# Performance work log

Measured on AMD Instinct MI355X. Metric: run time of the kernel, lower is better.

The kernel has to match this reference:

```python
import jax, jax.numpy as jnp
import numpy as np

NEG_BIG = -2.0**32 + 1.0  # padding value used by the torch module


def setup_inputs() -> dict:
    key = jax.random.key(0)
    k1, k2, k3, k4 = jax.random.split(key, 4)
    B, T, D = 8, 1024, 1024
    x = jax.random.normal(k1, (B, T, D), dtype=jnp.float32)
    mask = jnp.ones((B, T), dtype=jnp.float32)
    Wq = jax.random.normal(k2, (D, D), dtype=jnp.float32) * 0.02
    Wk = jax.random.normal(k3, (D, D), dtype=jnp.float32) * 0.02
    Wv = jax.random.normal(k4, (D, D), dtype=jnp.float32) * 0.02
    return {"x": x, "mask": mask, "Wq": Wq, "Wk": Wk, "Wv": Wv}


def reference(x, mask, Wq, Wk, Wv):
    # direction = FORWARD, dropout = 0.0, n_heads = 8
    n_heads = 8
    B, T, D = x.shape
    d = D // n_heads

    # nn.Linear(bias=False): y = x @ W.T
    Q = x @ Wq.T
    K = x @ Wk.T
    V = x @ Wv.T

    # torch.cat(torch.split(Q, d, dim=2), dim=0) -> [h*B, T, d], head-major
    def heads(t):
        return t.reshape(B, T, n_heads, d).transpose(2, 0, 1, 3)  # (h,B,T,d)

    Qh, Kh, Vh = heads(Q), heads(K), heads(V)

    scores = jnp.einsum('hbqd,hbkd->hbqk', Qh, Kh) / jnp.sqrt(jnp.float32(d))

    # key padding mask from K_ itself
    key_masks = jnp.sign(jnp.sum(jnp.abs(Kh), axis=-1))  # (h,B,T)
    scores = jnp.where(key_masks[:, :, None, :] == 0, jnp.float32(NEG_BIG), scores)

    # FORWARD direction: sw_col[i,j]=i, sw_row[i,j]=j; mask = (j > i) -> strict upper tri
    dir_mask = jnp.triu(jnp.ones((T, T), dtype=jnp.float32), k=1)
    adder = (1.0 - dir_mask) * -10000.0
    scores = scores + adder  # broadcasts over (h,B)

    attn = jax.nn.softmax(scores, axis=-1)

    query_masks = jnp.sign(jnp.sum(jnp.abs(Qh), axis=-1))  # (h,B,T)
    attn = attn * query_masks[:, :, :, None]

    out = jnp.einsum('hbqk,hbkd->hbqd', attn, Vh)  # (h,B,T,d)
    out = out.transpose(1, 2, 0, 3).reshape(B, T, D)  # cat heads back on feature dim

    out = out * mask[:, :, None]
    return out
```

## Files before the change

### kernel.cpp

```cpp
#include <hip/hip_runtime.h>
#include <hip/hip_bf16.h>
#include <stdint.h>


typedef __attribute__((ext_vector_type(8))) short short8;
typedef __attribute__((ext_vector_type(4))) float floatx4;

__device__ __forceinline__ short f2bf(float f) {
    union { float f; uint32_t u; } v; v.f = f;
    uint32_t r = v.u + 0x7fffu + ((v.u >> 16) & 1u);
    return (short)(r >> 16);
}

__device__ __forceinline__ void load_lds_16B(const void* g, void* l) {
    __builtin_amdgcn_global_load_lds(
        (const __attribute__((address_space(1))) void*)g,
        (__attribute__((address_space(3))) void*)l, 16, 0, 0);
}

__global__ __launch_bounds__(256) void cast_kernel(
    const float* __restrict__ src, short* __restrict__ dst, int n8)
{
    int i = blockIdx.x * 256 + threadIdx.x;
    if (i >= n8) return;
    float4 a = *(const float4*)(src + i * 8);
    float4 b = *(const float4*)(src + i * 8 + 4);
    short8 o;
    o[0] = f2bf(a.x); o[1] = f2bf(a.y); o[2] = f2bf(a.z); o[3] = f2bf(a.w);
    o[4] = f2bf(b.x); o[5] = f2bf(b.y); o[6] = f2bf(b.z); o[7] = f2bf(b.w);
    *(short8*)(dst + i * 8) = o;
}

__global__ __launch_bounds__(256) void cast3_kernel(
    const float* __restrict__ w0, const float* __restrict__ w1,
    const float* __restrict__ w2, short* __restrict__ dst)
{
    int sel = blockIdx.x >> 9;
    int blk = blockIdx.x & 511;
    const float* src = (sel == 0) ? w0 : ((sel == 1) ? w1 : w2);
    int i = blk * 256 + threadIdx.x;
    float4 a = *(const float4*)(src + i * 8);
    float4 b = *(const float4*)(src + i * 8 + 4);
    short8 o;
    o[0] = f2bf(a.x); o[1] = f2bf(a.y); o[2] = f2bf(a.z); o[3] = f2bf(a.w);
    o[4] = f2bf(b.x); o[5] = f2bf(b.y); o[6] = f2bf(b.z); o[7] = f2bf(b.w);
    *(short8*)(dst + sel * 1048576 + i * 8) = o;
}

__global__ __launch_bounds__(256) void qkv_gemm_kernel(
    const short* __restrict__ xb, const short* __restrict__ wb,
    short* __restrict__ Qh, short* __restrict__ Kh, short* __restrict__ VhT)
{
    __shared__ short As[2][4096];
    __shared__ short Bs[2][4096];
    __shared__ short Cs[8704];

    const int tid = threadIdx.x;
    const int m0 = blockIdx.y * 128;
    const int n0 = blockIdx.x * 128;
    const int wave = tid >> 6;
    const int lane = tid & 63;
    const int wm = (wave >> 1) * 64;
    const int wn = (wave & 1) * 64;
    const int l16 = lane & 15;
    const int quad = lane >> 4;
    const int srow = lane >> 2;
    const int scol = (lane & 3) * 8;

    floatx4 zero = {0.0f, 0.0f, 0.0f, 0.0f};
    floatx4 acc[4][4];
    for (int i = 0; i < 4; ++i)
        for (int j = 0; j < 4; ++j) acc[i][j] = zero;

    auto stage = [&](int k0, int bf) {
        #pragma unroll
        for (int c = 0; c < 4; ++c) {
            int chunk = wave * 4 + c;
            if (chunk < 8)
                load_lds_16B(xb + (m0 + chunk * 16 + srow) * 1024 + k0 + scol,
                             &As[bf][chunk * 512]);
            else
                load_lds_16B(wb + (n0 + (chunk - 8) * 16 + srow) * 1024 + k0 + scol,
                             &Bs[bf][(chunk - 8) * 512]);
        }
    };

    stage(0, 0);
    int buf = 0;
    for (int k0 = 0; k0 < 1024; k0 += 32) {
        __syncthreads();
        if (k0 + 32 < 1024) stage(k0 + 32, buf ^ 1);

        short8 a[4], b[4];
        #pragma unroll
        for (int i = 0; i < 4; ++i)
            a[i] = *(const short8*)&As[buf][(wm + i * 16 + l16) * 32 + quad * 8];
        #pragma unroll
        for (int j = 0; j < 4; ++j)
            b[j] = *(const short8*)&Bs[buf][(wn + j * 16 + l16) * 32 + quad * 8];
        #pragma unroll
        for (int i = 0; i < 4; ++i)
            #pragma unroll
            for (int j = 0; j < 4; ++j)
                acc[i][j] = __builtin_amdgcn_mfma_f32_16x16x32_bf16(a[i], b[j], acc[i][j], 0, 0, 0);
        buf ^= 1;
    }

    const float qscale = 0.08838834764831845f;
    const int f0 = n0 & 1023;
    const int h = f0 >> 7;
    const bool isV = (n0 >= 2048);
    const float sc = (n0 < 1024) ? qscale : 1.0f;
    short* dst = (n0 < 1024) ? Qh : Kh;

    #pragma unroll
    for (int half = 0; half < 2; ++half) {
        __syncthreads();
        if ((wave >> 1) == half) {
            #pragma unroll
            for (int i = 0; i < 4; ++i)
                #pragma unroll
                for (int j = 0; j < 4; ++j)
                    #pragma unroll
                    for (int p = 0; p < 4; ++p) {
                        int mr = i * 16 + quad * 4 + p;
                        int c = wn + j * 16 + l16;
                        short v = f2bf(acc[i][j][p] * sc);
                        if (isV) Cs[c * 68 + mr] = v;
                        else     Cs[mr * 132 + c] = v;
                    }
        }
        __syncthreads();
        if (!isV) {
            #pragma unroll
            for (int jj = 0; jj < 4; ++jj) {
                int idx = tid + jj * 256;
                int row = idx >> 4;
                int chunk = idx & 15;
                int m = m0 + half * 64 + row;
                int bb = m >> 10, t = m & 1023;
                *(short8*)&dst[((h * 8 + bb) * 1024 + t) * 128 + chunk * 8] =
                    *(const short8*)&Cs[row * 132 + chunk * 8];
            }
        } else {
            int m = m0 + half * 64;
            int bb = m >> 10, t = m & 1023;
            #pragma unroll
            for (int jj = 0; jj < 4; ++jj) {
                int idx = tid + jj * 256;
                int dd = idx >> 3;
                int chunk = idx & 7;
                *(short8*)&VhT[((h * 8 + bb) * 128 + dd) * 1024 + t + chunk * 8] =
                    *(const short8*)&Cs[dd * 68 + chunk * 8];
            }
        }
    }
}

#define LDP 70

__global__ __launch_bounds__(256) void attn_kernel(
    const short* __restrict__ Qh, const short* __restrict__ Kh,
    const short* __restrict__ VhT, const float* __restrict__ mask,
    float* __restrict__ out)
{
    __shared__ short Kb[2][8192];
    __shared__ short Vb[2][8192];
    __shared__ short Ps[4 * 16 * LDP];

    const int tid = threadIdx.x;
    const int qt = blockIdx.x;
    const int hb = blockIdx.y;
    const int h = hb >> 3, b = hb & 7;

    const int wave = tid >> 6;
    const int lane = tid & 63;
    const int l16 = lane & 15;
    const int quad = lane >> 4;

    const int base = hb * 131072;
    const short* Qp = Qh + base;
    const short* Kp = Kh + base;
    const short* VTp = VhT + base;
    short* Pw = &Ps[wave * 16 * LDP];

    const int q0_lo = qt * 64 + wave * 16;
    const int q0_hi = (15 - qt) * 64 + wave * 16;
    const int hi_start = 15 - qt;
    const bool hi_all = (qt == 0) && (wave == 3);

    short8 aq_lo[4], aq_hi[4];
    #pragma unroll
    for (int kk = 0; kk < 4; ++kk) {
        aq_lo[kk] = *(const short8*)(Qp + (q0_lo + l16) * 128 + kk * 32 + quad * 8);
        aq_hi[kk] = *(const short8*)(Qp + (q0_hi + l16) * 128 + kk * 32 + quad * 8);
    }

    floatx4 zero = {0.0f, 0.0f, 0.0f, 0.0f};
    floatx4 o_lo[8], o_hi[8];
    #pragma unroll
    for (int n = 0; n < 8; ++n) { o_lo[n] = zero; o_hi[n] = zero; }
    float l_lo[4] = {0, 0, 0, 0}, l_hi[4] = {0, 0, 0, 0};

    auto stage = [&](int kt, int bf) {
        #pragma unroll
        for (int c = 0; c < 4; ++c) {
            int L = wave * 4 + c;
            int kk = L >> 2, rg = L & 3;
            load_lds_16B(Kp + (kt * 64 + rg * 16 + (lane >> 2)) * 128 + kk * 32 + (lane & 3) * 8,
                         &Kb[bf][kk * 2048 + rg * 512]);
        }
        #pragma unroll
        for (int c = 0; c < 4; ++c) {
            int L = wave * 4 + c;
            int kk2 = L >> 3, g = L & 7;
            load_lds_16B(VTp + (g * 16 + (lane >> 2)) * 1024 + kt * 64 + kk2 * 32 + (lane & 3) * 8,
                         &Vb[bf][kk2 * 4096 + g * 512]);
        }
    };

    auto process = [&](int bf, int kt, const short8* aq, floatx4* o, float* l, int q0g) {
        floatx4 s[4];
        #pragma unroll
        for (int sub = 0; sub < 4; ++sub) {
            s[sub] = zero;
            #pragma unroll
            for (int kk = 0; kk < 4; ++kk) {
                short8 bk = *(const short8*)&Kb[bf][kk * 2048 + (sub * 16 + l16) * 32 + quad * 8];
                s[sub] = __builtin_amdgcn_mfma_f32_16x16x32_bf16(aq[kk], bk, s[sub], 0, 0, 0);
            }
        }
        #pragma unroll
        for (int sub = 0; sub < 4; ++sub)
            #pragma unroll
            for (int p = 0; p < 4; ++p) {
                int qg = q0g + quad * 4 + p;
                int kg = kt * 64 + sub * 16 + l16;
                float sv = s[sub][p];
                if (kg <= qg && qg != 1023) sv -= 10000.0f;
                float e = __expf(sv);
                l[p] += e;
                Pw[(quad * 4 + p) * LDP + sub * 16 + l16] = f2bf(e);
            }
        #pragma unroll
        for (int kk2 = 0; kk2 < 2; ++kk2) {
            short8 ap = *(const short8*)&Pw[l16 * LDP + kk2 * 32 + quad * 8];
            #pragma unroll
            for (int n = 0; n < 8; ++n) {
                short8 bv = *(const short8*)&Vb[bf][kk2 * 4096 + (n * 16 + l16) * 32 + quad * 8];
                o[n] = __builtin_amdgcn_mfma_f32_16x16x32_bf16(ap, bv, o[n], 0, 0, 0);
            }
        }
    };

    stage(qt, 0);
    int buf = 0;
    for (int kt = qt; kt < 16; ++kt) {
        __syncthreads();
        if (kt + 1 < 16) stage(kt + 1, buf ^ 1);
        process(buf, kt, aq_lo, o_lo, l_lo, q0_lo);
        if (kt >= hi_start || hi_all)
            process(buf, kt, aq_hi, o_hi, l_hi, q0_hi);
        buf ^= 1;
    }

    #pragma unroll
    for (int off = 8; off >= 1; off >>= 1)
        #pragma unroll
        for (int p = 0; p < 4; ++p) {
            l_lo[p] += __shfl_xor(l_lo[p], off);
            l_hi[p] += __shfl_xor(l_hi[p], off);
        }

    #pragma unroll
    for (int p = 0; p < 4; ++p) {
        int qg = q0_lo + quad * 4 + p;
        float s = (1.0f / l_lo[p]) * mask[b * 1024 + qg];
        #pragma unroll
        for (int n = 0; n < 8; ++n)
            out[(b * 1024 + qg) * 1024 + h * 128 + n * 16 + l16] = o_lo[n][p] * s;
    }
    #pragma unroll
    for (int p = 0; p < 4; ++p) {
        int qg = q0_hi + quad * 4 + p;
        float s = (1.0f / l_hi[p]) * mask[b * 1024 + qg];
        #pragma unroll
        for (int n = 0; n < 8; ++n)
            out[(b * 1024 + qg) * 1024 + h * 128 + n * 16 + l16] = o_hi[n][p] * s;
    }
}

extern "C" void kernel_launch(void* const* d_in, const int* in_sizes, int n_in,
                              void* d_out, int out_size, void* d_ws, size_t ws_size,
                              hipStream_t stream) {
    const float* x    = (const float*)d_in[0];
    const float* mask = (const float*)d_in[1];
    const float* Wq   = (const float*)d_in[2];
    const float* Wk   = (const float*)d_in[3];
    const float* Wv   = (const float*)d_in[4];
    float* out = (float*)d_out;

    short* xb  = (short*)d_ws;
    short* wb  = xb + 8388608;
    short* Qh  = wb + 3145728;
    short* Kh  = Qh + 8388608;
    short* VhT = Kh + 8388608;

    cast_kernel<<<4096, 256, 0, stream>>>(x, xb, 1048576);
    cast3_kernel<<<1536, 256, 0, stream>>>(Wq, Wk, Wv, wb);
    qkv_gemm_kernel<<<dim3(24, 64), 256, 0, stream>>>(xb, wb, Qh, Kh, VhT);
    attn_kernel<<<dim3(8, 64), 256, 0, stream>>>(Qh, Kh, VhT, mask, out);
}
```

Before: 262.1 us.

## Fuse cast kernels, swap grid axes, interleave attention phases, split out last row

Merges the two fp32-to-bf16 cast launches into one kernel. Swaps grid dimensions for the GEMM and attention kernels, which changes block scheduling order and cache locality. Splits each attention tile step into separate score, exp and PV phases and interleaves the lo and hi query tiles so MFMA work can overlap the exponential math. The special all-keys case for query row 1023 moves out of the main attention kernel into a small dedicated kernel, removing the divergent hi_all path at the cost of one extra launch that overwrites that row.

Result: faster. 247.2 us (-5.7%).

```diff
diff --git a/kernel.cpp b/kernel.cpp
--- a/kernel.cpp
+++ b/kernel.cpp
@@ -11,6 +11,10 @@
     uint32_t r = v.u + 0x7fffu + ((v.u >> 16) & 1u);
     return (short)(r >> 16);
 }
+__device__ __forceinline__ float bf2f(short u) {
+    union { float f; uint32_t x; } v; v.x = ((uint32_t)(uint16_t)u) << 16;
+    return v.f;
+}
 
 __device__ __forceinline__ void load_lds_16B(const void* g, void* l) {
     __builtin_amdgcn_global_load_lds(
@@ -18,33 +22,30 @@
         (__attribute__((address_space(3))) void*)l, 16, 0, 0);
 }
 
-__global__ __launch_bounds__(256) void cast_kernel(
-    const float* __restrict__ src, short* __restrict__ dst, int n8)
+__global__ __launch_bounds__(256) void cast_all_kernel(
+    const float* __restrict__ x, const float* __restrict__ w0,
+    const float* __restrict__ w1, const float* __restrict__ w2,
+    short* __restrict__ xb, short* __restrict__ wb)
 {
-    int i = blockIdx.x * 256 + threadIdx.x;
-    if (i >= n8) return;
+    int bid = blockIdx.x;
+    const float* src;
+    short* dst;
+    int i;
+    if (bid < 4096) {
+        src = x; dst = xb; i = bid * 256 + threadIdx.x;
+    } else {
+        int sel = (bid - 4096) >> 9;
+        int blk = (bid - 4096) & 511;
+        src = (sel == 0) ? w0 : ((sel == 1) ? w1 : w2);
+        dst = wb + sel * 1048576;
+        i = blk * 256 + threadIdx.x;
+    }
     float4 a = *(const float4*)(src + i * 8);
     float4 b = *(const float4*)(src + i * 8 + 4);
     short8 o;
     o[0] = f2bf(a.x); o[1] = f2bf(a.y); o[2] = f2bf(a.z); o[3] = f2bf(a.w);
     o[4] = f2bf(b.x); o[5] = f2bf(b.y); o[6] = f2bf(b.z); o[7] = f2bf(b.w);
     *(short8*)(dst + i * 8) = o;
-}
-
-__global__ __launch_bounds__(256) void cast3_kernel(
-    const float* __restrict__ w0, const float* __restrict__ w1,
-    const float* __restrict__ w2, short* __restrict__ dst)
-{
-    int sel = blockIdx.x >> 9;
-    int blk = blockIdx.x & 511;
-    const float* src = (sel == 0) ? w0 : ((sel == 1) ? w1 : w2);
-    int i = blk * 256 + threadIdx.x;
-    float4 a = *(const float4*)(src + i * 8);
-    float4 b = *(const float4*)(src + i * 8 + 4);
-    short8 o;
-    o[0] = f2bf(a.x); o[1] = f2bf(a.y); o[2] = f2bf(a.z); o[3] = f2bf(a.w);
-    o[4] = f2bf(b.x); o[5] = f2bf(b.y); o[6] = f2bf(b.z); o[7] = f2bf(b.w);
-    *(short8*)(dst + sel * 1048576 + i * 8) = o;
 }
 
 __global__ __launch_bounds__(256) void qkv_gemm_kernel(
@@ -56,8 +57,8 @@
     __shared__ short Cs[8704];
 
     const int tid = threadIdx.x;
-    const int m0 = blockIdx.y * 128;
-    const int n0 = blockIdx.x * 128;
+    const int m0 = blockIdx.x * 128;
+    const int n0 = blockIdx.y * 128;
     const int wave = tid >> 6;
     const int lane = tid & 63;
     const int wm = (wave >> 1) * 64;
@@ -169,8 +170,8 @@
     __shared__ short Ps[4 * 16 * LDP];
 
     const int tid = threadIdx.x;
-    const int qt = blockIdx.x;
-    const int hb = blockIdx.y;
+    const int hb = blockIdx.x;
+    const int qt = blockIdx.y;
     const int h = hb >> 3, b = hb & 7;
 
     const int wave = tid >> 6;
@@ -187,7 +188,6 @@
     const int q0_lo = qt * 64 + wave * 16;
     const int q0_hi = (15 - qt) * 64 + wave * 16;
     const int hi_start = 15 - qt;
-    const bool hi_all = (qt == 0) && (wave == 3);
 
     short8 aq_lo[4], aq_hi[4];
     #pragma unroll
@@ -219,8 +219,7 @@
         }
     };
 
-    auto process = [&](int bf, int kt, const short8* aq, floatx4* o, float* l, int q0g) {
-        floatx4 s[4];
+    auto s_phase = [&](int bf, const short8* aq, floatx4* s) {
         #pragma unroll
         for (int sub = 0; sub < 4; ++sub) {
             s[sub] = zero;
@@ -230,6 +229,8 @@
                 s[sub] = __builtin_amdgcn_mfma_f32_16x16x32_bf16(aq[kk], bk, s[sub], 0, 0, 0);
             }
         }
+    };
+    auto exp_phase = [&](floatx4* s, int q0g, float* l, int kt) {
         #pragma unroll
         for (int sub = 0; sub < 4; ++sub)
             #pragma unroll
@@ -242,6 +243,8 @@
                 l[p] += e;
                 Pw[(quad * 4 + p) * LDP + sub * 16 + l16] = f2bf(e);
             }
+    };
+    auto pv_phase = [&](int bf, floatx4* o) {
         #pragma unroll
         for (int kk2 = 0; kk2 < 2; ++kk2) {
             short8 ap = *(const short8*)&Pw[l16 * LDP + kk2 * 32 + quad * 8];
@@ -258,9 +261,16 @@
     for (int kt = qt; kt < 16; ++kt) {
         __syncthreads();
         if (kt + 1 < 16) stage(kt + 1, buf ^ 1);
-        process(buf, kt, aq_lo, o_lo, l_lo, q0_lo);
-        if (kt >= hi_start || hi_all)
-            process(buf, kt, aq_hi, o_hi, l_hi, q0_hi);
+        const bool do_hi = (kt >= hi_start);
+        floatx4 s_lo[4], s_hi[4];
+        s_phase(buf, aq_lo, s_lo);
+        exp_phase(s_lo, q0_lo, l_lo, kt);
+        if (do_hi) s_phase(buf, aq_hi, s_hi);
+        pv_phase(buf, o_lo);
+        if (do_hi) {
+            exp_phase(s_hi, q0_hi, l_hi, kt);
+            pv_phase(buf, o_hi);
+        }
         buf ^= 1;
     }
 
@@ -288,6 +298,61 @@
         for (int n = 0; n < 8; ++n)
             out[(b * 1024 + qg) * 1024 + h * 128 + n * 16 + l16] = o_hi[n][p] * s;
     }
+}
+
+__global__ __launch_bounds__(256) void row1023_kernel(
+    const short* __restrict__ Qh, const short* __restrict__ Kh,
+    const short* __restrict__ VhT, const float* __restrict__ mask,
+    float* __restrict__ out)
+{
+    __shared__ float qv[128];
+    __shared__ float ps[1024];
+    __shared__ float red[4];
+
+    const int hb = blockIdx.x;
+    const int h = hb >> 3, b = hb & 7;
+    const int base = hb * 131072;
+    const int tid = threadIdx.x;
+    const int wave = tid >> 6, lane = tid & 63;
+
+    if (tid < 128) qv[tid] = bf2f(Qh[base + 1023 * 128 + tid]);
+    __syncthreads();
+
+    float tot = 0.0f;
+    #pragma unroll
+    for (int kk = 0; kk < 4; ++kk) {
+        int k = tid * 4 + kk;
+        const short8* kr = (const short8*)(Kh + base + k * 128);
+        float acc = 0.0f;
+        #pragma unroll
+        for (int c = 0; c < 16; ++c) {
+            short8 v = kr[c];
+            #pragma unroll
+            for (int j = 0; j < 8; ++j) acc += qv[c * 8 + j] * bf2f(v[j]);
+        }
+        float e = __expf(acc);
+        ps[k] = e;
+        tot += e;
+    }
+    #pragma unroll
+    for (int off = 32; off >= 1; off >>= 1) tot += __shfl_xor(tot, off);
+    if (lane == 0) red[wave] = tot;
+    __syncthreads();
+    float inv = 1.0f / (red[0] + red[1] + red[2] + red[3]);
+    inv *= mask[b * 1024 + 1023];
+
+    int dd = tid >> 1, half = tid & 1;
+    const short* vr = VhT + base + dd * 1024 + half * 512;
+    const float* pp = ps + half * 512;
+    float acc = 0.0f;
+    for (int k = 0; k < 512; k += 8) {
+        short8 v = *(const short8*)(vr + k);
+        #pragma unroll
+        for (int j = 0; j < 8; ++j) acc += pp[k + j] * bf2f(v[j]);
+    }
+    acc += __shfl_xor(acc, 1);
+    if (half == 0)
+        out[(b * 1024 + 1023) * 1024 + h * 128 + dd] = acc * inv;
 }
 
 extern "C" void kernel_launch(void* const* d_in, const int* in_sizes, int n_in,
@@ -306,8 +371,8 @@
     short* Kh  = Qh + 8388608;
     short* VhT = Kh + 8388608;
 
-    cast_kernel<<<4096, 256, 0, stream>>>(x, xb, 1048576);
-    cast3_kernel<<<1536, 256, 0, stream>>>(Wq, Wk, Wv, wb);
-    qkv_gemm_kernel<<<dim3(24, 64), 256, 0, stream>>>(xb, wb, Qh, Kh, VhT);
-    attn_kernel<<<dim3(8, 64), 256, 0, stream>>>(Qh, Kh, VhT, mask, out);
-}
+    cast_all_kernel<<<5632, 256, 0, stream>>>(x, Wq, Wk, Wv, xb, wb);
+    qkv_gemm_kernel<<<dim3(64, 24), 256, 0, stream>>>(xb, wb, Qh, Kh, VhT);
+    attn_kernel<<<dim3(64, 8), 256, 0, stream>>>(Qh, Kh, VhT, mask, out);
+    row1023_kernel<<<64, 256, 0, stream>>>(Qh, Kh, VhT, mask, out);
+}
```
